# Performance work log

Hardware: AMD Instinct MI355X
Metric: run time of the kernel (lower is better)

## Reference

```python
import jax, jax.numpy as jnp
import numpy as np


def setup_inputs() -> dict:
    key = jax.random.key(0)
    k1, k2, k3 = jax.random.split(key, 3)
    B, H, S, D = 4, 16, 1024, 64
    return {
        "query": jax.random.normal(k1, (B, H, S, D), dtype=jnp.float32),
        "key": jax.random.normal(k2, (B, H, D, S), dtype=jnp.float32),  # pre-transposed K
        "scale_factor": 8,  # sqrt(head_dim)
        "attention_mask": jnp.zeros((S, S), dtype=jnp.float32),
        "value": jax.random.normal(k3, (B, H, S, D), dtype=jnp.float32),
    }


def reference(query, key, scale_factor, attention_mask, value):
    # Batched equivalent of the per-(b,h) Python loop:
    # scores = Q @ K^T / scale + mask; probs = softmax(scores); out = probs @ V
    scores = jnp.matmul(query, key) / scale_factor  # [B,H,S,S]
    if attention_mask is not None:
        scores = scores + attention_mask  # broadcast [S,S] over [B,H,S,S]
    probs = jax.nn.softmax(scores, axis=-1)
    return jnp.matmul(probs, value)  # [B,H,S,D]
```

## Files before the change

kernel.cpp:

```cpp
#include <hip/hip_runtime.h>

#define BH  64
#define SEQ 1024
#define DIM 64
#define KT  64
#define NT  (SEQ / KT)

typedef __attribute__((ext_vector_type(8))) short  short8;
typedef __attribute__((ext_vector_type(4))) float  floatx4;
typedef __attribute__((ext_vector_type(4))) uint   uintx4;

__device__ __forceinline__ ushort f2bf(float x) {
    union { float f; uint u; } v; v.f = x;
    uint r = v.u + 0x7FFFu + ((v.u >> 16) & 1u);
    return (ushort)(r >> 16);
}
__device__ __forceinline__ uint pack2(float lo, float hi) {
    return (uint)f2bf(lo) | ((uint)f2bf(hi) << 16);
}
__device__ __forceinline__ uint pk2(float lo, float hi) {
    union { float f; uint u; } a, b; a.f = lo; b.f = hi;
    uint au = a.u + 0x8000u, bu = b.u + 0x8000u;
    return __builtin_amdgcn_perm(bu, au, 0x07060302);
}
__device__ __forceinline__ void gld_lds16(const void* g, void* l) {
    __builtin_amdgcn_global_load_lds(
        (const __attribute__((address_space(1))) unsigned int*)g,
        (__attribute__((address_space(3))) unsigned int*)l, 16, 0, 0);
}


__global__ __launch_bounds__(256) void prep_kv_kernel(
    const float* __restrict__ Kin,
    const float* __restrict__ Vin,
    ushort* __restrict__ Kbf, ushort* __restrict__ Vbf)
{
    __shared__ float tile[64][65];
    const int t    = threadIdx.x;
    const int head = blockIdx.y;
    const int s0   = blockIdx.x * 64;
    const int p    = t & 7;

    if (blockIdx.z == 0) {
        const float* ip = Kin + (size_t)head * DIM * SEQ;
#pragma unroll
        for (int i = 0; i < 4; ++i) {
            const int d = (t >> 4) + i * 16;
            const int c = (t & 15) * 4;
            float4 v = *(const float4*)(ip + (size_t)d * SEQ + s0 + c);
            tile[d][c]     = v.x; tile[d][c + 1] = v.y;
            tile[d][c + 2] = v.z; tile[d][c + 3] = v.w;
        }
        __syncthreads();
        char* op = (char*)(Kbf + (size_t)head * SEQ * DIM);
#pragma unroll
        for (int i = 0; i < 2; ++i) {
            const int s  = (t >> 3) + i * 32;
            const int dg = (p ^ (s & 7)) * 8;
            uint4 wv;
            wv.x = pack2(tile[dg + 0][s], tile[dg + 1][s]);
            wv.y = pack2(tile[dg + 2][s], tile[dg + 3][s]);
            wv.z = pack2(tile[dg + 4][s], tile[dg + 5][s]);
            wv.w = pack2(tile[dg + 6][s], tile[dg + 7][s]);
            *(uint4*)(op + (size_t)(s0 + s) * 128 + p * 16) = wv;
        }
    } else {
        const float* ip = Vin + (size_t)head * SEQ * DIM;
#pragma unroll
        for (int i = 0; i < 4; ++i) {
            const int ss = (t >> 4) + i * 16;
            const int c  = (t & 15) * 4;
            float4 v = *(const float4*)(ip + (size_t)(s0 + ss) * DIM + c);
            tile[ss][c]     = v.x; tile[ss][c + 1] = v.y;
            tile[ss][c + 2] = v.z; tile[ss][c + 3] = v.w;
        }
        __syncthreads();
        char* op = (char*)(Vbf + (size_t)head * SEQ * DIM) + (size_t)(s0 >> 6) * 8192;
#pragma unroll
        for (int i = 0; i < 2; ++i) {
            const int d  = (t >> 3) + i * 32;
            const int g  = p ^ (d & 7);
            const int kb = ((g >> 2) * 32) + ((g & 3) * 4);
            uint4 wv;
            wv.x = pack2(tile[kb +  0][d], tile[kb +  1][d]);
            wv.y = pack2(tile[kb +  2][d], tile[kb +  3][d]);
            wv.z = pack2(tile[kb + 16][d], tile[kb + 17][d]);
            wv.w = pack2(tile[kb + 18][d], tile[kb + 19][d]);
            *(uint4*)(op + (size_t)d * 128 + p * 16) = wv;
        }
    }
}

__global__ __launch_bounds__(256) void prep_maskT_kernel(
    const float* __restrict__ m, float* __restrict__ mt)
{
    __shared__ float tile[32][33];
    const int t  = threadIdx.x;
    const int k0 = blockIdx.x * 32;
    const int q0 = blockIdx.y * 32;
    const int tx = t & 31, ty = t >> 5;
#pragma unroll
    for (int i = 0; i < 4; ++i)
        tile[ty + 8 * i][tx] = m[(size_t)(q0 + ty + 8 * i) * SEQ + k0 + tx];
    __syncthreads();
#pragma unroll
    for (int i = 0; i < 4; ++i)
        mt[(size_t)(k0 + ty + 8 * i) * SEQ + q0 + tx] = tile[tx][ty + 8 * i];
}

__global__ __launch_bounds__(512, 4) void mha_mfma2_kernel(
    const float*  __restrict__ Q,
    const ushort* __restrict__ Kbf,
    const int*    __restrict__ scale_p,
    const float*  __restrict__ maskT,
    const ushort* __restrict__ Vbf,
    float*        __restrict__ O)
{
    __shared__ __align__(16) ushort Ks0[KT * 64], Ks1[KT * 64];
    __shared__ __align__(16) ushort Vt0[DIM * 64], Vt1[DIM * 64];

    const int t    = threadIdx.x;
    const int lane = t & 63, w = t >> 6;
    const int li   = lane & 15, quad = lane >> 4;
    const int lx   = li & 7;
    const int bh   = blockIdx.x >> 3;
    const int q0   = (blockIdx.x & 7) * 128;

    const float inv_scale = 1.0f / (float)scale_p[0];

    short8 qa0, qa1;
    {
        const float* Qr = Q + ((size_t)bh * SEQ + q0 + w * 16 + li) * DIM + quad * 8;
        float4 a = *(const float4*)(Qr);
        float4 b = *(const float4*)(Qr + 4);
        float4 c = *(const float4*)(Qr + 32);
        float4 d = *(const float4*)(Qr + 36);
        qa0 = __builtin_bit_cast(short8,
              uintx4{pack2(a.x, a.y), pack2(a.z, a.w), pack2(b.x, b.y), pack2(b.z, b.w)});
        qa1 = __builtin_bit_cast(short8,
              uintx4{pack2(c.x, c.y), pack2(c.z, c.w), pack2(d.x, d.y), pack2(d.z, d.w)});
    }

    floatx4 o[4] = {floatx4{0,0,0,0}, floatx4{0,0,0,0},
                    floatx4{0,0,0,0}, floatx4{0,0,0,0}};
    float l = 0.f;

    const char* KgH = (const char*)(Kbf + (size_t)bh * SEQ * DIM);
    const char* VgH = (const char*)(Vbf + (size_t)bh * SEQ * DIM);
    const int so = w * 1024 + lane * 16;
    char* ksd0 = (char*)Ks0 + w * 1024;
    char* ksd1 = (char*)Ks1 + w * 1024;
    char* vtd0 = (char*)Vt0 + w * 1024;
    char* vtd1 = (char*)Vt1 + w * 1024;

    const float* mrowT = maskT + (size_t)(quad * 4) * SEQ + q0 + w * 16 + li;

    float mvc[16], mvn[16];
#pragma unroll
    for (int n = 0; n < 4; ++n)
#pragma unroll
        for (int r = 0; r < 4; ++r)
            mvc[n * 4 + r] = mrowT[(size_t)(n * 16 + r) * SEQ];
    gld_lds16(KgH + so, ksd0);
    gld_lds16(VgH + so, vtd0);
    __builtin_amdgcn_sched_barrier(0);

#pragma unroll 2
    for (int kt = 0; kt < NT; ++kt) {
        const int c = kt & 1;
        const char* ksb = c ? (const char*)Ks1 : (const char*)Ks0;
        const char* vtb = c ? (const char*)Vt1 : (const char*)Vt0;
        char* ksdN = c ? ksd0 : ksd1;
        char* vtdN = c ? vtd0 : vtd1;

        __builtin_amdgcn_s_barrier();

        const int kn = (kt + 1) & (NT - 1);
#pragma unroll
        for (int n = 0; n < 4; ++n)
#pragma unroll
            for (int r = 0; r < 4; ++r)
                mvn[n * 4 + r] = mrowT[(size_t)(kn * KT + n * 16 + r) * SEQ];
        gld_lds16(KgH + kn * 8192 + so, ksdN);
        gld_lds16(VgH + kn * 8192 + so, vtdN);
        __builtin_amdgcn_sched_barrier(0);
        asm volatile("s_waitcnt vmcnt(18)" ::: "memory");
        __builtin_amdgcn_sched_barrier(0);
        __builtin_amdgcn_s_barrier();

        floatx4 cfr[4] = {floatx4{0,0,0,0}, floatx4{0,0,0,0},
                          floatx4{0,0,0,0}, floatx4{0,0,0,0}};
        __builtin_amdgcn_s_setprio(1);
#pragma unroll
        for (int n = 0; n < 4; ++n) {
            const char* krow = ksb + (n * 16 + li) * 128;
            short8 kf0 = *(const short8*)(krow + ((quad ^ lx) * 16));
            short8 kf1 = *(const short8*)(krow + (((4 + quad) ^ lx) * 16));
            cfr[n] = __builtin_amdgcn_mfma_f32_16x16x32_bf16(kf0, qa0, cfr[n], 0, 0, 0);
            cfr[n] = __builtin_amdgcn_mfma_f32_16x16x32_bf16(kf1, qa1, cfr[n], 0, 0, 0);
        }
        __builtin_amdgcn_s_setprio(0);

        uint pw[8];
#pragma unroll
        for (int n = 0; n < 4; ++n) {
            float p0 = __expf(fminf(fmaf(cfr[n][0], inv_scale, mvc[n * 4 + 0]), 80.f));
            float p1 = __expf(fminf(fmaf(cfr[n][1], inv_scale, mvc[n * 4 + 1]), 80.f));
            float p2 = __expf(fminf(fmaf(cfr[n][2], inv_scale, mvc[n * 4 + 2]), 80.f));
            float p3 = __expf(fminf(fmaf(cfr[n][3], inv_scale, mvc[n * 4 + 3]), 80.f));
            l += ((p0 + p1) + (p2 + p3));
            pw[n * 2]     = pk2(p0, p1);
            pw[n * 2 + 1] = pk2(p2, p3);
        }
        const short8 pa0 = __builtin_bit_cast(short8, uintx4{pw[0], pw[1], pw[2], pw[3]});
        const short8 pa1 = __builtin_bit_cast(short8, uintx4{pw[4], pw[5], pw[6], pw[7]});

        __builtin_amdgcn_s_setprio(1);
#pragma unroll
        for (int n = 0; n < 4; ++n) {
            const char* vrow = vtb + (n * 16 + li) * 128;
            short8 b0 = *(const short8*)(vrow + ((quad ^ lx) * 16));
            short8 b1 = *(const short8*)(vrow + (((4 + quad) ^ lx) * 16));
            o[n] = __builtin_amdgcn_mfma_f32_16x16x32_bf16(pa0, b0, o[n], 0, 0, 0);
            o[n] = __builtin_amdgcn_mfma_f32_16x16x32_bf16(pa1, b1, o[n], 0, 0, 0);
        }
        __builtin_amdgcn_s_setprio(0);

#pragma unroll
        for (int j = 0; j < 16; ++j) mvc[j] = mvn[j];
    }

    l += __shfl_xor(l, 16);
    l += __shfl_xor(l, 32);
    float linv[4];
#pragma unroll
    for (int r = 0; r < 4; ++r)
        linv[r] = 1.0f / __shfl(l, quad * 4 + r);

    float* Og = O + ((size_t)bh * SEQ + q0) * DIM;
#pragma unroll
    for (int r = 0; r < 4; ++r) {
#pragma unroll
        for (int n = 0; n < 4; ++n)
            Og[(size_t)(w * 16 + quad * 4 + r) * DIM + n * 16 + li] = o[n][r] * linv[r];
    }
}

extern "C" void kernel_launch(void* const* d_in, const int* in_sizes, int n_in,
                              void* d_out, int out_size, void* d_ws, size_t ws_size,
                              hipStream_t stream) {
    const float* Q     = (const float*)d_in[0];
    const float* K     = (const float*)d_in[1];
    const int*   scale = (const int*)d_in[2];
    const float* mask  = (const float*)d_in[3];
    const float* V     = (const float*)d_in[4];
    float*       Out   = (float*)d_out;

    ushort* Kbf   = (ushort*)d_ws;
    ushort* Vbf   = Kbf + (size_t)BH * SEQ * DIM;
    float*  maskT = (float*)((char*)d_ws + 2 * (size_t)BH * SEQ * DIM * 2);

    prep_kv_kernel<<<dim3(SEQ / 64, BH, 2), 256, 0, stream>>>(K, V, Kbf, Vbf);
    prep_maskT_kernel<<<dim3(SEQ / 32, SEQ / 32), 256, 0, stream>>>(mask, maskT);
    mha_mfma2_kernel<<<dim3(BH * (SEQ / 128)), 512, 0, stream>>>(Q, Kbf, scale, maskT, Vbf, Out);
}
```

Before: 134.9 us.

## Double the key tile to 128 and load mask values inside the loop

Raises the key/value tile from 64 to 128 keys per iteration, which halves the loop trip count and the barriers per tile and doubles the LDS staging per buffer. The mask prefetch into registers for the next tile is dropped. Mask values are now loaded for the current tile after the barrier, and the vmcnt wait is adjusted to match. This cuts synchronisation overhead per key and frees registers, but exposes mask load latency, raises LDS use (which may lower occupancy), and adds more live registers for eight score fragments.

```diff
diff --git a/kernel.cpp b/kernel.cpp
--- a/kernel.cpp
+++ b/kernel.cpp
@@ -3,7 +3,7 @@
 #define BH  64
 #define SEQ 1024
 #define DIM 64
-#define KT  64
+#define KT  128
 #define NT  (SEQ / KT)
 
 typedef __attribute__((ext_vector_type(8))) short  short8;
@@ -117,7 +117,7 @@
     float*        __restrict__ O)
 {
     __shared__ __align__(16) ushort Ks0[KT * 64], Ks1[KT * 64];
-    __shared__ __align__(16) ushort Vt0[DIM * 64], Vt1[DIM * 64];
+    __shared__ __align__(16) ushort Vt0[DIM * KT], Vt1[DIM * KT];
 
     const int t    = threadIdx.x;
     const int lane = t & 63, w = t >> 6;
@@ -147,22 +147,18 @@
 
     const char* KgH = (const char*)(Kbf + (size_t)bh * SEQ * DIM);
     const char* VgH = (const char*)(Vbf + (size_t)bh * SEQ * DIM);
-    const int so = w * 1024 + lane * 16;
-    char* ksd0 = (char*)Ks0 + w * 1024;
-    char* ksd1 = (char*)Ks1 + w * 1024;
-    char* vtd0 = (char*)Vt0 + w * 1024;
-    char* vtd1 = (char*)Vt1 + w * 1024;
+    const int so = w * 2048 + lane * 16;
+    char* ksd0 = (char*)Ks0 + w * 2048;
+    char* ksd1 = (char*)Ks1 + w * 2048;
+    char* vtd0 = (char*)Vt0 + w * 2048;
+    char* vtd1 = (char*)Vt1 + w * 2048;
 
     const float* mrowT = maskT + (size_t)(quad * 4) * SEQ + q0 + w * 16 + li;
 
-    float mvc[16], mvn[16];
-#pragma unroll
-    for (int n = 0; n < 4; ++n)
-#pragma unroll
-        for (int r = 0; r < 4; ++r)
-            mvc[n * 4 + r] = mrowT[(size_t)(n * 16 + r) * SEQ];
-    gld_lds16(KgH + so, ksd0);
-    gld_lds16(VgH + so, vtd0);
+    gld_lds16(KgH + so,        ksd0);
+    gld_lds16(KgH + so + 1024, ksd0 + 1024);
+    gld_lds16(VgH + so,        vtd0);
+    gld_lds16(VgH + so + 1024, vtd0 + 1024);
     __builtin_amdgcn_sched_barrier(0);
 
 #pragma unroll 2
@@ -176,23 +172,33 @@
         __builtin_amdgcn_s_barrier();
 
         const int kn = (kt + 1) & (NT - 1);
-#pragma unroll
-        for (int n = 0; n < 4; ++n)
-#pragma unroll
-            for (int r = 0; r < 4; ++r)
-                mvn[n * 4 + r] = mrowT[(size_t)(kn * KT + n * 16 + r) * SEQ];
-        gld_lds16(KgH + kn * 8192 + so, ksdN);
-        gld_lds16(VgH + kn * 8192 + so, vtdN);
+        {
+            const char* kg = KgH + kn * 16384 + so;
+            const char* vg = VgH + kn * 16384 + so;
+            gld_lds16(kg,        ksdN);
+            gld_lds16(kg + 1024, ksdN + 1024);
+            gld_lds16(vg,        vtdN);
+            gld_lds16(vg + 1024, vtdN + 1024);
+        }
         __builtin_amdgcn_sched_barrier(0);
-        asm volatile("s_waitcnt vmcnt(18)" ::: "memory");
+        asm volatile("s_waitcnt vmcnt(4)" ::: "memory");
         __builtin_amdgcn_sched_barrier(0);
         __builtin_amdgcn_s_barrier();
 
-        floatx4 cfr[4] = {floatx4{0,0,0,0}, floatx4{0,0,0,0},
-                          floatx4{0,0,0,0}, floatx4{0,0,0,0}};
+        float mv[32];
+#pragma unroll
+        for (int n = 0; n < 8; ++n)
+#pragma unroll
+            for (int r = 0; r < 4; ++r)
+                mv[n * 4 + r] = mrowT[(size_t)(kt * KT + n * 16 + r) * SEQ];
+        __builtin_amdgcn_sched_barrier(0);
+
+        floatx4 cfr[8];
+#pragma unroll
+        for (int n = 0; n < 8; ++n) cfr[n] = floatx4{0, 0, 0, 0};
         __builtin_amdgcn_s_setprio(1);
 #pragma unroll
-        for (int n = 0; n < 4; ++n) {
+        for (int n = 0; n < 8; ++n) {
             const char* krow = ksb + (n * 16 + li) * 128;
             short8 kf0 = *(const short8*)(krow + ((quad ^ lx) * 16));
             short8 kf1 = *(const short8*)(krow + (((4 + quad) ^ lx) * 16));
@@ -201,19 +207,21 @@
         }
         __builtin_amdgcn_s_setprio(0);
 
-        uint pw[8];
-#pragma unroll
-        for (int n = 0; n < 4; ++n) {
-            float p0 = __expf(fminf(fmaf(cfr[n][0], inv_scale, mvc[n * 4 + 0]), 80.f));
-            float p1 = __expf(fminf(fmaf(cfr[n][1], inv_scale, mvc[n * 4 + 1]), 80.f));
-            float p2 = __expf(fminf(fmaf(cfr[n][2], inv_scale, mvc[n * 4 + 2]), 80.f));
-            float p3 = __expf(fminf(fmaf(cfr[n][3], inv_scale, mvc[n * 4 + 3]), 80.f));
+        uint pw[16];
+#pragma unroll
+        for (int n = 0; n < 8; ++n) {
+            float p0 = __expf(fminf(fmaf(cfr[n][0], inv_scale, mv[n * 4 + 0]), 80.f));
+            float p1 = __expf(fminf(fmaf(cfr[n][1], inv_scale, mv[n * 4 + 1]), 80.f));
+            float p2 = __expf(fminf(fmaf(cfr[n][2], inv_scale, mv[n * 4 + 2]), 80.f));
+            float p3 = __expf(fminf(fmaf(cfr[n][3], inv_scale, mv[n * 4 + 3]), 80.f));
             l += ((p0 + p1) + (p2 + p3));
             pw[n * 2]     = pk2(p0, p1);
             pw[n * 2 + 1] = pk2(p2, p3);
         }
-        const short8 pa0 = __builtin_bit_cast(short8, uintx4{pw[0], pw[1], pw[2], pw[3]});
-        const short8 pa1 = __builtin_bit_cast(short8, uintx4{pw[4], pw[5], pw[6], pw[7]});
+        const short8 pa0 = __builtin_bit_cast(short8, uintx4{pw[0],  pw[1],  pw[2],  pw[3]});
+        const short8 pa1 = __builtin_bit_cast(short8, uintx4{pw[4],  pw[5],  pw[6],  pw[7]});
+        const short8 pa2 = __builtin_bit_cast(short8, uintx4{pw[8],  pw[9],  pw[10], pw[11]});
+        const short8 pa3 = __builtin_bit_cast(short8, uintx4{pw[12], pw[13], pw[14], pw[15]});
 
         __builtin_amdgcn_s_setprio(1);
 #pragma unroll
@@ -224,10 +232,15 @@
             o[n] = __builtin_amdgcn_mfma_f32_16x16x32_bf16(pa0, b0, o[n], 0, 0, 0);
             o[n] = __builtin_amdgcn_mfma_f32_16x16x32_bf16(pa1, b1, o[n], 0, 0, 0);
         }
+#pragma unroll
+        for (int n = 0; n < 4; ++n) {
+            const char* vrow = vtb + 8192 + (n * 16 + li) * 128;
+            short8 b0 = *(const short8*)(vrow + ((quad ^ lx) * 16));
+            short8 b1 = *(const short8*)(vrow + (((4 + quad) ^ lx) * 16));
+            o[n] = __builtin_amdgcn_mfma_f32_16x16x32_bf16(pa2, b0, o[n], 0, 0, 0);
+            o[n] = __builtin_amdgcn_mfma_f32_16x16x32_bf16(pa3, b1, o[n], 0, 0, 0);
+        }
         __builtin_amdgcn_s_setprio(0);
-
-#pragma unroll
-        for (int j = 0; j < 16; ++j) mvc[j] = mvn[j];
     }
 
     l += __shfl_xor(l, 16);
```

Measured after the change: 134.0 us. About the same (-0.7%).
